# Performance work log

Hardware: AMD Instinct MI355X
Metric: run time of the kernel (lower is better)

Reference implementation:

```python
import jax, jax.numpy as jnp
import numpy as np

# Grid config: output_shape = [2, 40, 400, 352, 16] -> sparse_shape = [41, 400, 352]
B, Dz, Hy, Wx = 2, 41, 400, 352
N_PER = 20000          # active voxels per sample
C_IN = 128
# Strided SparseConv3d(k=3, s=2, p=1) output spatial dims
Do, Ho, Wo = (Dz + 2 - 3) // 2 + 1, (Hy + 2 - 3) // 2 + 1, (Wx + 2 - 3) // 2 + 1


def setup_inputs() -> dict:
    rng = np.random.default_rng(0)
    coors_list = []
    for b in range(B):
        # unique voxel positions per sample (z limited to original 40-deep grid)
        flat = rng.choice((Dz - 1) * Hy * Wx, size=N_PER, replace=False)
        z = flat // (Hy * Wx)
        r = flat % (Hy * Wx)
        y = r // Wx
        x = r % Wx
        coors_list.append(np.stack([np.full(N_PER, b), z, y, x], axis=1))
    coors = jnp.asarray(np.concatenate(coors_list, 0), jnp.int32)  # [N,4]

    key = jax.random.key(0)
    k1, k2, k3, k4 = jax.random.split(key, 4)
    N = B * N_PER
    voxel_features = jax.random.normal(k1, (N, C_IN), jnp.float32)
    W1 = jax.random.normal(k2, (3, 3, 3, C_IN, 16), jnp.float32) * (1.0 / np.sqrt(27 * C_IN))
    W2 = jax.random.normal(k3, (3, 3, 3, 16, 16), jnp.float32) * (1.0 / np.sqrt(27 * 16))
    W3 = jax.random.normal(k4, (3, 3, 3, 16, 32), jnp.float32) * (1.0 / np.sqrt(27 * 16))
    return dict(voxel_features=voxel_features, coors=coors, W1=W1, W2=W2, W3=W3, batch_size=B)


def _offsets():
    o = jnp.stack(jnp.meshgrid(jnp.arange(3), jnp.arange(3), jnp.arange(3), indexing='ij'), -1)
    return o.reshape(27, 3)  # [27,3] kernel taps


def reference(voxel_features, coors, W1, W2, W3, batch_size):
    N = voxel_features.shape[0]
    offs = _offsets()

    # --- rulebook: dense index grid, padded by 1 so neighbor lookups never go OOB
    grid = jnp.full((batch_size, Dz + 2, Hy + 2, Wx + 2), -1, jnp.int32)
    grid = grid.at[coors[:, 0], coors[:, 1] + 1, coors[:, 2] + 1, coors[:, 3] + 1].set(
        jnp.arange(N, dtype=jnp.int32))
    # neighbor voxel index for every active site and every 3x3x3 tap: [N,27]
    nbr = grid[coors[:, 0:1], coors[:, 1:2] + offs[:, 0], coors[:, 2:3] + offs[:, 1],
               coors[:, 3:4] + offs[:, 2]]
    valid = (nbr >= 0)[..., None]
    nbr_c = jnp.clip(nbr, 0, N - 1)

    def subm(feat, W):  # submanifold conv: gather -> GEMM, output only on active sites
        Cin, Cout = W.shape[3], W.shape[4]
        g = jnp.where(valid, feat[nbr_c], 0.0)                      # [N,27,Cin]
        return jnp.einsum('nkc,kcd->nd', g, W.reshape(27, Cin, Cout))

    x = jax.nn.relu(subm(voxel_features, W1))   # SubMConv3d(128->16) + ReLU
    x = jax.nn.relu(subm(x, W2))                # SubMConv3d(16->16, same rulebook) + ReLU

    # --- SparseConv3d(16->32, k=3, stride=2, pad=1): scatter-add into downsampled grid
    contrib = jnp.einsum('nc,kcd->nkd', x, W3.reshape(27, 16, 32))  # [N,27,32]
    oz = coors[:, 1:2] + 1 - offs[:, 0]  # p_in + pad - k, must be even and in range
    oy = coors[:, 2:3] + 1 - offs[:, 1]
    ox = coors[:, 3:4] + 1 - offs[:, 2]
    pz, py, px = oz // 2, oy // 2, ox // 2
    ok = ((oz % 2 == 0) & (oy % 2 == 0) & (ox % 2 == 0) &
          (pz >= 0) & (pz < Do) & (py >= 0) & (py < Ho) & (px >= 0) & (px < Wo))
    total = batch_size * Do * Ho * Wo
    flat = coors[:, 0:1] * (Do * Ho * Wo) + pz * (Ho * Wo) + py * Wo + px
    flat = jnp.where(ok, flat, total)  # invalid -> dummy slot
    out = jnp.zeros((total + 1, 32), x.dtype).at[flat.reshape(-1)].add(
        contrib.reshape(-1, 32))[:total]
    out = jax.nn.relu(out).reshape(batch_size, Do, Ho, Wo, 32)  # dense() of sparse output
    return out
```

## Files before the change

kernel.cpp:

```cpp
#include <hip/hip_runtime.h>

#define B_   2
#define DZ   41
#define HY   400
#define WX   352
#define NVOX 40000
#define PD   43
#define PH   402
#define PW   354
#define DO_  21
#define HO_  200
#define WO_  176
#define C1   128
#define GRID_CELLS (B_*PD*PH*PW)
#define OUT_ELEMS  (B_*DO_*HO_*WO_*32)
#define OUT_F4     (OUT_ELEMS/4)
#define GRID_F4    (GRID_CELLS*2/16)


__global__ void k_zero4(float4* __restrict__ p, int n4) {
    int i = blockIdx.x * 256 + threadIdx.x;
    if (i < n4) p[i] = make_float4(0.f, 0.f, 0.f, 0.f);
}

__global__ void k_build(const int* __restrict__ coors, unsigned short* __restrict__ grid) {
    int n = blockIdx.x * blockDim.x + threadIdx.x;
    if (n >= NVOX) return;
    int b = coors[4*n+0], z = coors[4*n+1], y = coors[4*n+2], x = coors[4*n+3];
    grid[((b*PD + z+1)*PH + y+1)*PW + x+1] = (unsigned short)(n + 1);
}

__global__ void k_nbrc(const int* __restrict__ coors, const unsigned short* __restrict__ grid,
                       int* __restrict__ nbrc) {
    int n = blockIdx.x * 256 + threadIdx.x;
    if (n >= NVOX) return;
    int b = coors[4*n+0], z = coors[4*n+1], y = coors[4*n+2], x = coors[4*n+3];
    int* dst = nbrc + n * 28;
    int cnt = 0;
    for (int k = 0; k < 27; ++k) {
        int dz = k / 9, dy = (k / 3) % 3, dx = k % 3;
        int id = (int)grid[((b*PD + z+dz)*PH + y+dy)*PW + x+dx] - 1;
        if (id >= 0) dst[1 + cnt++] = (k << 16) | id;
    }
    dst[0] = cnt;
}

__global__ void k_subm1(const float* __restrict__ feat,
                        const float* __restrict__ W1,
                        const int* __restrict__ nbrc, float* __restrict__ x1) {
    __shared__ int s_p[16][28];
    int base = blockIdx.x * 16;
    for (int i = threadIdx.x; i < 16*28; i += 256) {
        int v = i / 28, j = i % 28;
        int n = base + v;
        s_p[v][j] = (n < NVOX) ? nbrc[n*28 + j] : 0;
    }
    __syncthreads();
    int v = threadIdx.x >> 4, d = threadIdx.x & 15;
    int n = base + v;
    if (n >= NVOX) return;
    int cnt = s_p[v][0];
    float acc = 0.f;
    for (int t = 1; t <= cnt; ++t) {
        int pk = s_p[v][t];
        int k = pk >> 16, idx = pk & 0xFFFF;
        const float4* f4 = (const float4*)(feat + (size_t)idx * C1);
        const float* w = W1 + k * (C1*16) + d;
        #pragma unroll 8
        for (int c4 = 0; c4 < 32; ++c4) {
            float4 f = f4[c4];
            acc += f.x * w[(c4*4+0)*16];
            acc += f.y * w[(c4*4+1)*16];
            acc += f.z * w[(c4*4+2)*16];
            acc += f.w * w[(c4*4+3)*16];
        }
    }
    x1[n*16 + d] = fmaxf(acc, 0.f);
}

__global__ void k_subm2(const float* __restrict__ x1,
                        const float* __restrict__ W2,
                        const int* __restrict__ nbrc, float* __restrict__ x2) {
    __shared__ int s_p[16][28];
    int base = blockIdx.x * 16;
    for (int i = threadIdx.x; i < 16*28; i += 256) {
        int v = i / 28, j = i % 28;
        int n = base + v;
        s_p[v][j] = (n < NVOX) ? nbrc[n*28 + j] : 0;
    }
    __syncthreads();
    int v = threadIdx.x >> 4, d = threadIdx.x & 15;
    int n = base + v;
    if (n >= NVOX) return;
    int cnt = s_p[v][0];
    float acc = 0.f;
    for (int t = 1; t <= cnt; ++t) {
        int pk = s_p[v][t];
        int k = pk >> 16, idx = pk & 0xFFFF;
        const float4* xr = (const float4*)(x1 + (size_t)idx * 16);
        float4 a0 = xr[0], a1 = xr[1], a2 = xr[2], a3 = xr[3];
        const float* w = W2 + k * 256 + d;
        acc += a0.x*w[0*16]  + a0.y*w[1*16]  + a0.z*w[2*16]  + a0.w*w[3*16]
             + a1.x*w[4*16]  + a1.y*w[5*16]  + a1.z*w[6*16]  + a1.w*w[7*16]
             + a2.x*w[8*16]  + a2.y*w[9*16]  + a2.z*w[10*16] + a2.w*w[11*16]
             + a3.x*w[12*16] + a3.y*w[13*16] + a3.z*w[14*16] + a3.w*w[15*16];
    }
    x2[n*16 + d] = fmaxf(acc, 0.f);
}

__device__ __forceinline__ int axis_taps(int pcoord, int outdim, int* ds, int* ps) {
    if (pcoord & 1) { ds[0] = 1; ps[0] = pcoord >> 1; return 1; }
    int h = pcoord >> 1, nu = 0;
    if (h < outdim) { ds[nu] = 0; ps[nu] = h; nu++; }
    ds[nu] = 2; ps[nu] = h - 1; nu++;
    return nu;
}

__global__ void k_scatter(const float* __restrict__ x2,
                          const float* __restrict__ W3,
                          const int* __restrict__ coors,
                          float* __restrict__ out) {
    int v = threadIdx.x >> 5, d = threadIdx.x & 31;
    int n = blockIdx.x * 8 + v;
    if (n >= NVOX) return;
    int b  = coors[4*n+0];
    int zp = coors[4*n+1] + 1, yp = coors[4*n+2] + 1, xp = coors[4*n+3] + 1;
    int dz[2], pz[2], dy[2], py[2], dx[2], px[2];
    int nz = axis_taps(zp, DO_, dz, pz);
    int ny = axis_taps(yp, HO_, dy, py);
    int nx = axis_taps(xp, WO_, dx, px);
    const float4* xr = (const float4*)(x2 + (size_t)n * 16);
    float r[16];
    *(float4*)(r + 0)  = xr[0];
    *(float4*)(r + 4)  = xr[1];
    *(float4*)(r + 8)  = xr[2];
    *(float4*)(r + 12) = xr[3];
    int bofs = b * (DO_*HO_*WO_);
    for (int iz = 0; iz < nz; ++iz)
        for (int iy = 0; iy < ny; ++iy)
            for (int ix = 0; ix < nx; ++ix) {
                int k = dz[iz]*9 + dy[iy]*3 + dx[ix];
                int p = bofs + (pz[iz]*HO_ + py[iy])*WO_ + px[ix];
                const float* w = W3 + k*512 + d;
                float acc = 0.f;
                #pragma unroll
                for (int c = 0; c < 16; ++c) acc += r[c] * w[c * 32];
                atomicAdd(out + (size_t)p * 32 + d, acc);
            }
}

__global__ void k_relu(const int* __restrict__ coors, float* __restrict__ out) {
    int v = threadIdx.x >> 5, d = threadIdx.x & 31;
    int n = blockIdx.x * 8 + v;
    if (n >= NVOX) return;
    int b  = coors[4*n+0];
    int zp = coors[4*n+1] + 1, yp = coors[4*n+2] + 1, xp = coors[4*n+3] + 1;
    int dz[2], pz[2], dy[2], py[2], dx[2], px[2];
    int nz = axis_taps(zp, DO_, dz, pz);
    int ny = axis_taps(yp, HO_, dy, py);
    int nx = axis_taps(xp, WO_, dx, px);
    int bofs = b * (DO_*HO_*WO_);
    for (int iz = 0; iz < nz; ++iz)
        for (int iy = 0; iy < ny; ++iy)
            for (int ix = 0; ix < nx; ++ix) {
                int p = bofs + (pz[iz]*HO_ + py[iy])*WO_ + px[ix];
                size_t o = (size_t)p * 32 + d;
                out[o] = fmaxf(out[o], 0.f);
            }
}

extern "C" void kernel_launch(void* const* d_in, const int* in_sizes, int n_in,
                              void* d_out, int out_size, void* d_ws, size_t ws_size,
                              hipStream_t stream) {
    const float* feat  = (const float*)d_in[0];
    const int*   coors = (const int*)d_in[1];
    const float* W1    = (const float*)d_in[2];
    const float* W2    = (const float*)d_in[3];
    const float* W3    = (const float*)d_in[4];
    float* out = (float*)d_out;

    char* ws = (char*)d_ws;
    size_t off = 0;
    unsigned short* grid = (unsigned short*)(ws + off);
    off += (((size_t)GRID_CELLS*2) + 255) & ~(size_t)255;
    int* nbrc = (int*)(ws + off); off += (((size_t)NVOX*28*4)  + 255) & ~(size_t)255;
    float* x1 = (float*)(ws + off); off += (((size_t)NVOX*16*4) + 255) & ~(size_t)255;
    float* x2 = (float*)(ws + off);

    k_zero4<<<(OUT_F4  + 255) / 256, 256, 0, stream>>>((float4*)out,  OUT_F4);
    k_zero4<<<(GRID_F4 + 255) / 256, 256, 0, stream>>>((float4*)grid, GRID_F4);
    k_build<<<(NVOX + 255) / 256, 256, 0, stream>>>(coors, grid);
    k_nbrc<<<(NVOX + 255) / 256, 256, 0, stream>>>(coors, grid, nbrc);
    k_subm1<<<(NVOX + 15) / 16, 256, 0, stream>>>(feat, W1, nbrc, x1);
    k_subm2<<<(NVOX + 15) / 16, 256, 0, stream>>>(x1, W2, nbrc, x2);
    k_scatter<<<(NVOX + 7) / 8, 256, 0, stream>>>(x2, W3, coors, out);
    k_relu<<<(NVOX + 7) / 8, 256, 0, stream>>>(coors, out);
}
```

Before: 338.3 us.

## Replace atomic output scatter with output-stationary gather and fused ReLU

The strided conv now marks occupied output positions in a byte mask during grid build, then a per-output kernel gathers its contributing input voxels through the index grid and writes every output position, occupied or zero, with ReLU applied. This removes the separate zero fill of the output, the float atomics and the ReLU pass. Neighbor lists for the submanifold convs are rebuilt in shared memory per block instead of stored in a global rulebook. In exchange, the grid lookups are repeated in both subm kernels and a grid probe is done per occupied output.

```diff
diff --git a/kernel.cpp b/kernel.cpp
--- a/kernel.cpp
+++ b/kernel.cpp
@@ -12,57 +12,76 @@
 #define HO_  200
 #define WO_  176
 #define C1   128
+#define OPP  (DO_*HO_*WO_)
+#define OUT_POS (B_*OPP)
 #define GRID_CELLS (B_*PD*PH*PW)
-#define OUT_ELEMS  (B_*DO_*HO_*WO_*32)
-#define OUT_F4     (OUT_ELEMS/4)
-#define GRID_F4    (GRID_CELLS*2/16)
-
-
-__global__ void k_zero4(float4* __restrict__ p, int n4) {
+#define GRID_F4  (GRID_CELLS*2/16)
+#define OMASK_F4 (OUT_POS/16)
+
+
+__device__ __forceinline__ int axis_taps(int pcoord, int outdim, int* ds, int* ps) {
+    if (pcoord & 1) { ds[0] = 1; ps[0] = pcoord >> 1; return 1; }
+    int h = pcoord >> 1, nu = 0;
+    if (h < outdim) { ds[nu] = 0; ps[nu] = h; nu++; }
+    ds[nu] = 2; ps[nu] = h - 1; nu++;
+    return nu;
+}
+
+__global__ void k_zero(float4* __restrict__ g, float4* __restrict__ m) {
     int i = blockIdx.x * 256 + threadIdx.x;
-    if (i < n4) p[i] = make_float4(0.f, 0.f, 0.f, 0.f);
-}
-
-__global__ void k_build(const int* __restrict__ coors, unsigned short* __restrict__ grid) {
-    int n = blockIdx.x * blockDim.x + threadIdx.x;
-    if (n >= NVOX) return;
-    int b = coors[4*n+0], z = coors[4*n+1], y = coors[4*n+2], x = coors[4*n+3];
-    grid[((b*PD + z+1)*PH + y+1)*PW + x+1] = (unsigned short)(n + 1);
-}
-
-__global__ void k_nbrc(const int* __restrict__ coors, const unsigned short* __restrict__ grid,
-                       int* __restrict__ nbrc) {
+    float4 z = make_float4(0.f, 0.f, 0.f, 0.f);
+    if (i < GRID_F4)  g[i] = z;
+    if (i < OMASK_F4) m[i] = z;
+}
+
+__global__ void k_build(const int* __restrict__ coors, unsigned short* __restrict__ grid,
+                        unsigned char* __restrict__ omask) {
     int n = blockIdx.x * 256 + threadIdx.x;
     if (n >= NVOX) return;
     int b = coors[4*n+0], z = coors[4*n+1], y = coors[4*n+2], x = coors[4*n+3];
-    int* dst = nbrc + n * 28;
-    int cnt = 0;
-    for (int k = 0; k < 27; ++k) {
+    int zp = z + 1, yp = y + 1, xp = x + 1;
+    grid[((b*PD + zp)*PH + yp)*PW + xp] = (unsigned short)(n + 1);
+    int dz[2], pz[2], dy[2], py[2], dx[2], px[2];
+    int nz = axis_taps(zp, DO_, dz, pz);
+    int ny = axis_taps(yp, HO_, dy, py);
+    int nx = axis_taps(xp, WO_, dx, px);
+    int bofs = b * OPP;
+    for (int iz = 0; iz < nz; ++iz)
+        for (int iy = 0; iy < ny; ++iy)
+            for (int ix = 0; ix < nx; ++ix)
+                omask[bofs + (pz[iz]*HO_ + py[iy])*WO_ + px[ix]] = 1;
+}
+
+__global__ void k_subm1(const float* __restrict__ feat, const float* __restrict__ W1,
+                        const int* __restrict__ coors, const unsigned short* __restrict__ grid,
+                        float* __restrict__ x1) {
+    __shared__ int s_base[16];
+    __shared__ int s_cnt[16];
+    __shared__ int s_list[16][27];
+    int base = blockIdx.x * 16;
+    int t = threadIdx.x;
+    if (t < 16) {
+        int n = base + t;
+        int b = coors[4*n+0], z = coors[4*n+1], y = coors[4*n+2], x = coors[4*n+3];
+        s_base[t] = ((b*PD + z)*PH + y)*PW + x;
+        s_cnt[t] = 0;
+    }
+    __syncthreads();
+    for (int i = t; i < 16*27; i += 256) {
+        int v = i / 27, k = i % 27;
         int dz = k / 9, dy = (k / 3) % 3, dx = k % 3;
-        int id = (int)grid[((b*PD + z+dz)*PH + y+dy)*PW + x+dx] - 1;
-        if (id >= 0) dst[1 + cnt++] = (k << 16) | id;
-    }
-    dst[0] = cnt;
-}
-
-__global__ void k_subm1(const float* __restrict__ feat,
-                        const float* __restrict__ W1,
-                        const int* __restrict__ nbrc, float* __restrict__ x1) {
-    __shared__ int s_p[16][28];
-    int base = blockIdx.x * 16;
-    for (int i = threadIdx.x; i < 16*28; i += 256) {
-        int v = i / 28, j = i % 28;
-        int n = base + v;
-        s_p[v][j] = (n < NVOX) ? nbrc[n*28 + j] : 0;
-    }
-    __syncthreads();
-    int v = threadIdx.x >> 4, d = threadIdx.x & 15;
-    int n = base + v;
-    if (n >= NVOX) return;
-    int cnt = s_p[v][0];
+        int id = (int)grid[s_base[v] + dz*(PH*PW) + dy*PW + dx] - 1;
+        if (id >= 0) {
+            int pos = atomicAdd(&s_cnt[v], 1);
+            s_list[v][pos] = (k << 16) | id;
+        }
+    }
+    __syncthreads();
+    int v = t >> 4, d = t & 15;
+    int cnt = s_cnt[v];
     float acc = 0.f;
-    for (int t = 1; t <= cnt; ++t) {
-        int pk = s_p[v][t];
+    for (int tap = 0; tap < cnt; ++tap) {
+        int pk = s_list[v][tap];
         int k = pk >> 16, idx = pk & 0xFFFF;
         const float4* f4 = (const float4*)(feat + (size_t)idx * C1);
         const float* w = W1 + k * (C1*16) + d;
@@ -75,27 +94,39 @@
             acc += f.w * w[(c4*4+3)*16];
         }
     }
-    x1[n*16 + d] = fmaxf(acc, 0.f);
-}
-
-__global__ void k_subm2(const float* __restrict__ x1,
-                        const float* __restrict__ W2,
-                        const int* __restrict__ nbrc, float* __restrict__ x2) {
-    __shared__ int s_p[16][28];
+    x1[(base + v)*16 + d] = fmaxf(acc, 0.f);
+}
+
+__global__ void k_subm2(const float* __restrict__ x1, const float* __restrict__ W2,
+                        const int* __restrict__ coors, const unsigned short* __restrict__ grid,
+                        float* __restrict__ x2) {
+    __shared__ int s_base[16];
+    __shared__ int s_cnt[16];
+    __shared__ int s_list[16][27];
     int base = blockIdx.x * 16;
-    for (int i = threadIdx.x; i < 16*28; i += 256) {
-        int v = i / 28, j = i % 28;
-        int n = base + v;
-        s_p[v][j] = (n < NVOX) ? nbrc[n*28 + j] : 0;
-    }
-    __syncthreads();
-    int v = threadIdx.x >> 4, d = threadIdx.x & 15;
-    int n = base + v;
-    if (n >= NVOX) return;
-    int cnt = s_p[v][0];
+    int t = threadIdx.x;
+    if (t < 16) {
+        int n = base + t;
+        int b = coors[4*n+0], z = coors[4*n+1], y = coors[4*n+2], x = coors[4*n+3];
+        s_base[t] = ((b*PD + z)*PH + y)*PW + x;
+        s_cnt[t] = 0;
+    }
+    __syncthreads();
+    for (int i = t; i < 16*27; i += 256) {
+        int v = i / 27, k = i % 27;
+        int dz = k / 9, dy = (k / 3) % 3, dx = k % 3;
+        int id = (int)grid[s_base[v] + dz*(PH*PW) + dy*PW + dx] - 1;
+        if (id >= 0) {
+            int pos = atomicAdd(&s_cnt[v], 1);
+            s_list[v][pos] = (k << 16) | id;
+        }
+    }
+    __syncthreads();
+    int v = t >> 4, d = t & 15;
+    int cnt = s_cnt[v];
     float acc = 0.f;
-    for (int t = 1; t <= cnt; ++t) {
-        int pk = s_p[v][t];
+    for (int tap = 0; tap < cnt; ++tap) {
+        int pk = s_list[v][tap];
         int k = pk >> 16, idx = pk & 0xFFFF;
         const float4* xr = (const float4*)(x1 + (size_t)idx * 16);
         float4 a0 = xr[0], a1 = xr[1], a2 = xr[2], a3 = xr[3];
@@ -105,68 +136,62 @@
              + a2.x*w[8*16]  + a2.y*w[9*16]  + a2.z*w[10*16] + a2.w*w[11*16]
              + a3.x*w[12*16] + a3.y*w[13*16] + a3.z*w[14*16] + a3.w*w[15*16];
     }
-    x2[n*16 + d] = fmaxf(acc, 0.f);
-}
-
-__device__ __forceinline__ int axis_taps(int pcoord, int outdim, int* ds, int* ps) {
-    if (pcoord & 1) { ds[0] = 1; ps[0] = pcoord >> 1; return 1; }
-    int h = pcoord >> 1, nu = 0;
-    if (h < outdim) { ds[nu] = 0; ps[nu] = h; nu++; }
-    ds[nu] = 2; ps[nu] = h - 1; nu++;
-    return nu;
-}
-
-__global__ void k_scatter(const float* __restrict__ x2,
-                          const float* __restrict__ W3,
-                          const int* __restrict__ coors,
-                          float* __restrict__ out) {
-    int v = threadIdx.x >> 5, d = threadIdx.x & 31;
-    int n = blockIdx.x * 8 + v;
-    if (n >= NVOX) return;
-    int b  = coors[4*n+0];
-    int zp = coors[4*n+1] + 1, yp = coors[4*n+2] + 1, xp = coors[4*n+3] + 1;
-    int dz[2], pz[2], dy[2], py[2], dx[2], px[2];
-    int nz = axis_taps(zp, DO_, dz, pz);
-    int ny = axis_taps(yp, HO_, dy, py);
-    int nx = axis_taps(xp, WO_, dx, px);
-    const float4* xr = (const float4*)(x2 + (size_t)n * 16);
-    float r[16];
-    *(float4*)(r + 0)  = xr[0];
-    *(float4*)(r + 4)  = xr[1];
-    *(float4*)(r + 8)  = xr[2];
-    *(float4*)(r + 12) = xr[3];
-    int bofs = b * (DO_*HO_*WO_);
-    for (int iz = 0; iz < nz; ++iz)
-        for (int iy = 0; iy < ny; ++iy)
-            for (int ix = 0; ix < nx; ++ix) {
-                int k = dz[iz]*9 + dy[iy]*3 + dx[ix];
-                int p = bofs + (pz[iz]*HO_ + py[iy])*WO_ + px[ix];
-                const float* w = W3 + k*512 + d;
-                float acc = 0.f;
-                #pragma unroll
-                for (int c = 0; c < 16; ++c) acc += r[c] * w[c * 32];
-                atomicAdd(out + (size_t)p * 32 + d, acc);
+    x2[(base + v)*16 + d] = fmaxf(acc, 0.f);
+}
+
+__global__ void k_out(const float* __restrict__ x2, const float* __restrict__ W3,
+                      const unsigned short* __restrict__ grid,
+                      const unsigned char* __restrict__ omask,
+                      float4* __restrict__ out4) {
+    __shared__ int s_base[32];
+    __shared__ int s_cnt[32];
+    __shared__ int s_list[32][27];
+    __shared__ unsigned char s_occ[32];
+    int pbase = blockIdx.x * 32;
+    int t = threadIdx.x;
+    if (t < 32) {
+        int p = pbase + t;
+        s_occ[t] = omask[p];
+        s_cnt[t] = 0;
+        int b   = p / OPP,       rem = p - b * OPP;
+        int pz  = rem / (HO_*WO_), r2 = rem - pz * (HO_*WO_);
+        int py  = r2 / WO_,       px = r2 - py * WO_;
+        s_base[t] = ((b*PD + 2*pz)*PH + 2*py)*PW + 2*px;
+    }
+    __syncthreads();
+    for (int i = t; i < 32*27; i += 256) {
+        int v = i / 27;
+        if (!s_occ[v]) continue;
+        int k = i % 27;
+        int dz = k / 9, dy = (k / 3) % 3, dx = k % 3;
+        int id = (int)grid[s_base[v] + dz*(PH*PW) + dy*PW + dx] - 1;
+        if (id >= 0) {
+            int pos = atomicAdd(&s_cnt[v], 1);
+            s_list[v][pos] = (k << 16) | id;
+        }
+    }
+    __syncthreads();
+    int v = t >> 3, c4 = t & 7;
+    float4 acc = make_float4(0.f, 0.f, 0.f, 0.f);
+    if (s_occ[v]) {
+        int cnt = s_cnt[v];
+        for (int tap = 0; tap < cnt; ++tap) {
+            int pk = s_list[v][tap];
+            int k = pk >> 16, idx = pk & 0xFFFF;
+            const float*  xp = x2 + (size_t)idx * 16;
+            const float4* w4 = (const float4*)(W3 + k*512 + c4*4);
+            #pragma unroll
+            for (int c = 0; c < 16; ++c) {
+                float xv = xp[c];
+                float4 w = w4[c * 8];
+                acc.x += xv * w.x; acc.y += xv * w.y;
+                acc.z += xv * w.z; acc.w += xv * w.w;
             }
-}
-
-__global__ void k_relu(const int* __restrict__ coors, float* __restrict__ out) {
-    int v = threadIdx.x >> 5, d = threadIdx.x & 31;
-    int n = blockIdx.x * 8 + v;
-    if (n >= NVOX) return;
-    int b  = coors[4*n+0];
-    int zp = coors[4*n+1] + 1, yp = coors[4*n+2] + 1, xp = coors[4*n+3] + 1;
-    int dz[2], pz[2], dy[2], py[2], dx[2], px[2];
-    int nz = axis_taps(zp, DO_, dz, pz);
-    int ny = axis_taps(yp, HO_, dy, py);
-    int nx = axis_taps(xp, WO_, dx, px);
-    int bofs = b * (DO_*HO_*WO_);
-    for (int iz = 0; iz < nz; ++iz)
-        for (int iy = 0; iy < ny; ++iy)
-            for (int ix = 0; ix < nx; ++ix) {
-                int p = bofs + (pz[iz]*HO_ + py[iy])*WO_ + px[ix];
-                size_t o = (size_t)p * 32 + d;
-                out[o] = fmaxf(out[o], 0.f);
-            }
+        }
+        acc.x = fmaxf(acc.x, 0.f); acc.y = fmaxf(acc.y, 0.f);
+        acc.z = fmaxf(acc.z, 0.f); acc.w = fmaxf(acc.w, 0.f);
+    }
+    out4[(size_t)(pbase + v) * 8 + c4] = acc;
 }
 
 extern "C" void kernel_launch(void* const* d_in, const int* in_sizes, int n_in,
@@ -183,16 +208,14 @@
     size_t off = 0;
     unsigned short* grid = (unsigned short*)(ws + off);
     off += (((size_t)GRID_CELLS*2) + 255) & ~(size_t)255;
-    int* nbrc = (int*)(ws + off); off += (((size_t)NVOX*28*4)  + 255) & ~(size_t)255;
+    unsigned char* omask = (unsigned char*)(ws + off);
+    off += ((size_t)OUT_POS + 255) & ~(size_t)255;
     float* x1 = (float*)(ws + off); off += (((size_t)NVOX*16*4) + 255) & ~(size_t)255;
     float* x2 = (float*)(ws + off);
 
-    k_zero4<<<(OUT_F4  + 255) / 256, 256, 0, stream>>>((float4*)out,  OUT_F4);
-    k_zero4<<<(GRID_F4 + 255) / 256, 256, 0, stream>>>((float4*)grid, GRID_F4);
-    k_build<<<(NVOX + 255) / 256, 256, 0, stream>>>(coors, grid);
-    k_nbrc<<<(NVOX + 255) / 256, 256, 0, stream>>>(coors, grid, nbrc);
-    k_subm1<<<(NVOX + 15) / 16, 256, 0, stream>>>(feat, W1, nbrc, x1);
-    k_subm2<<<(NVOX + 15) / 16, 256, 0, stream>>>(x1, W2, nbrc, x2);
-    k_scatter<<<(NVOX + 7) / 8, 256, 0, stream>>>(x2, W3, coors, out);
-    k_relu<<<(NVOX + 7) / 8, 256, 0, stream>>>(coors, out);
-}
+    k_zero <<<(GRID_F4 + 255) / 256, 256, 0, stream>>>((float4*)grid, (float4*)omask);
+    k_build<<<(NVOX + 255) / 256, 256, 0, stream>>>(coors, grid, omask);
+    k_subm1<<<NVOX / 16, 256, 0, stream>>>(feat, W1, coors, grid, x1);
+    k_subm2<<<NVOX / 16, 256, 0, stream>>>(x1, W2, coors, grid, x2);
+    k_out  <<<OUT_POS / 32, 256, 0, stream>>>(x2, W3, grid, omask, (float4*)out);
+}
```

Result: no change. 341.0 us (+0.8%).
